# Kernel optimization log

Hardware: AMD Instinct MI355X
Metric: run time of the kernel (lower is better)

The kernel has to match this reference:

```python
import jax, jax.numpy as jnp
import numpy as np

B, N, DIM, H, DH = 8, 1024, 768, 12, 64
INNER = H * DH
SCALE = DH ** -0.5


def _bias_idx(n):
    # Reproduce the offset->id mapping from the torch __init__ loop:
    # offsets are first seen in row-major (p1, p2) order, so
    # id(0)=0, id(-k)=k (k=1..n-1), id(+k)=n-1+k.
    i = np.arange(n)[:, None]
    j = np.arange(n)[None, :]
    off = i - j
    idx = np.where(off <= 0, -off, n - 1 + off)
    return jnp.asarray(idx, dtype=jnp.int32)  # (n, n), values in [0, 2n-2]


def setup_inputs() -> dict:
    key = jax.random.key(0)
    ks = jax.random.split(key, 5)
    x = jax.random.normal(ks[0], (B, N, DIM), dtype=jnp.float32)
    w_qkv = jax.random.normal(ks[1], (DIM, 3 * INNER), dtype=jnp.float32) * (DIM ** -0.5)
    bias_table = jax.random.normal(ks[2], (H, 2 * N - 1), dtype=jnp.float32) * 0.02
    w_out = jax.random.normal(ks[3], (INNER, DIM), dtype=jnp.float32) * (INNER ** -0.5)
    b_out = jnp.zeros((DIM,), dtype=jnp.float32)
    bias_idx = _bias_idx(N)
    return {"x": x, "w_qkv": w_qkv, "bias_table": bias_table,
            "w_out": w_out, "b_out": b_out, "bias_idx": bias_idx}


def reference(x, w_qkv, bias_table, w_out, b_out, bias_idx):
    b, n, _ = x.shape
    qkv = x @ w_qkv  # (b, n, 3*inner)
    q, k, v = jnp.split(qkv, 3, axis=-1)
    def heads(t):
        return t.reshape(b, n, H, DH).transpose(0, 2, 1, 3)  # (b, h, n, d)
    q, k, v = heads(q), heads(k), heads(v)
    bias = bias_table[:, bias_idx]  # (h, n, n), gathered per-head relpos bias
    dots = jnp.einsum('bhid,bhjd->bhij', q, k) * SCALE + bias[None]
    attn = jax.nn.softmax(dots, axis=-1)
    out = jnp.einsum('bhij,bhjd->bhid', attn, v)
    out = out.transpose(0, 2, 1, 3).reshape(b, n, INNER)
    return out @ w_out + b_out
```

## Files before the change

kernel.cpp:

```cpp
#include <hip/hip_runtime.h>
#include <hip/hip_bf16.h>
#include <stdint.h>

typedef unsigned short u16;
typedef unsigned int u32;
typedef __bf16 bf16x8 __attribute__((ext_vector_type(8)));
typedef _Float16 f16x8 __attribute__((ext_vector_type(8)));
typedef _Float16 f16x4 __attribute__((ext_vector_type(4)));
typedef __fp16 v4hf __attribute__((ext_vector_type(4)));
typedef float f32x4 __attribute__((ext_vector_type(4)));
typedef unsigned short u16x4 __attribute__((ext_vector_type(4)));
typedef unsigned int u32x2 __attribute__((ext_vector_type(2)));

#define SEQ     1024
#define DIM     768
#define NH      12
#define QKV_LD  2304
#define LOG2E   1.4426950408889634f
#define C1      0.18033688f

__device__ __forceinline__ float bf2f(u16 u) {
    union { unsigned v; float f; } x; x.v = ((unsigned)u) << 16; return x.f;
}
__device__ __forceinline__ u16 f2bf(float f) {
    union { float f; unsigned v; } x; x.f = f;
    unsigned r = (x.v + 0x7FFFu + ((x.v >> 16) & 1u)) >> 16;
    return (u16)r;
}
__device__ __forceinline__ void store_out(u16* p, float v)  { *p = f2bf(v); }
__device__ __forceinline__ void store_out(float* p, float v){ *p = v; }

__device__ __forceinline__ void async16(void* lds, const void* g) {
    __builtin_amdgcn_global_load_lds(
        (const __attribute__((address_space(1))) unsigned*)(uintptr_t)g,
        (__attribute__((address_space(3))) unsigned*)(unsigned)(uintptr_t)lds,
        16, 0, 0);
}

__global__ __launch_bounds__(256) void cvt_k(const float* __restrict__ in,
                                             u16* __restrict__ out) {
    int i = (blockIdx.x * 256 + threadIdx.x) * 4;
    float4 v = *(const float4*)(in + i);
    u16x4 o = { f2bf(v.x), f2bf(v.y), f2bf(v.z), f2bf(v.w) };
    *(u16x4*)(out + i) = o;
}

__global__ __launch_bounds__(256) void transpose_k(const float* __restrict__ in,
                                                   u16* __restrict__ out,
                                                   int R, int C) {
    __shared__ __align__(16) float t[32][33];
    int c0 = blockIdx.x * 32, r0 = blockIdx.y * 32;
    int tx = threadIdx.x & 31, ty = threadIdx.x >> 5;
#pragma unroll
    for (int i = 0; i < 32; i += 8)
        t[ty + i][tx] = in[(size_t)(r0 + ty + i) * C + c0 + tx];
    __syncthreads();
#pragma unroll
    for (int i = 0; i < 32; i += 8)
        out[(size_t)(c0 + ty + i) * R + r0 + tx] = f2bf(t[tx][ty + i]);
}

__global__ __launch_bounds__(256) void vt_k(const u16* __restrict__ qkv,
                                            _Float16* __restrict__ vT) {
    __shared__ __align__(16) u16 t[32][33];
    int bh = blockIdx.z;
    int b = bh / 12, h = bh % 12;
    int key0 = blockIdx.x * 32, dh0 = blockIdx.y * 32;
    int tx = threadIdx.x & 31, ty = threadIdx.x >> 5;
#pragma unroll
    for (int i = 0; i < 32; i += 8)
        t[ty + i][tx] = qkv[(size_t)(b * SEQ + key0 + ty + i) * QKV_LD +
                            1536 + h * 64 + dh0 + tx];
    __syncthreads();
#pragma unroll
    for (int i = 0; i < 32; i += 8)
        vT[(size_t)(bh * 64 + dh0 + ty + i) * SEQ + key0 + tx] =
            (_Float16)bf2f(t[tx][ty + i]);
}

template <int HAS_BIAS, typename OUT_T>
__global__ __launch_bounds__(256) void gemm_bt(const u16* __restrict__ A,
                                               const u16* __restrict__ Bt,
                                               const float* __restrict__ bias,
                                               OUT_T* __restrict__ C,
                                               int M, int N, int K) {
    __shared__ __align__(16) u16 sA[128 * 64];
    __shared__ __align__(16) u16 sB[128 * 64];
    const int tid = threadIdx.x;
    const int lane = tid & 63;
    const int quad = lane >> 4, l16 = lane & 15;
    const int wave = tid >> 6;
    const int m0 = blockIdx.x * 128, n0 = blockIdx.y * 128;
    const int wm = (wave >> 1) * 64, wn = (wave & 1) * 64;

    const int co0 = (quad ^ (l16 & 7)) * 8;
    f32x4 acc[4][4] = {};

    for (int k0 = 0; k0 < K; k0 += 64) {
        __syncthreads();
#pragma unroll
        for (int rep = 0; rep < 4; ++rep) {
            int i = rep * 256 + tid;
            int row = i >> 3;
            int c = (i & 7) ^ (row & 7);
            async16(&sA[i * 8], A + (size_t)(m0 + row) * K + k0 + c * 8);
            async16(&sB[i * 8], Bt + (size_t)(n0 + row) * K + k0 + c * 8);
        }
        __syncthreads();

#pragma unroll
        for (int ks = 0; ks < 2; ++ks) {
            const int co = co0 ^ (ks * 32);
            bf16x8 af[4], bfr[4];
#pragma unroll
            for (int mi = 0; mi < 4; ++mi)
                af[mi] = *(const bf16x8*)&sA[(wm + mi * 16 + l16) * 64 + co];
#pragma unroll
            for (int nj = 0; nj < 4; ++nj)
                bfr[nj] = *(const bf16x8*)&sB[(wn + nj * 16 + l16) * 64 + co];
#pragma unroll
            for (int mi = 0; mi < 4; ++mi)
#pragma unroll
                for (int nj = 0; nj < 4; ++nj)
                    acc[mi][nj] = __builtin_amdgcn_mfma_f32_16x16x32_bf16(
                        af[mi], bfr[nj], acc[mi][nj], 0, 0, 0);
        }
    }

#pragma unroll
    for (int mi = 0; mi < 4; ++mi) {
#pragma unroll
        for (int nj = 0; nj < 4; ++nj) {
            int col = n0 + wn + nj * 16 + l16;
            float bv = HAS_BIAS ? bias[col] : 0.0f;
#pragma unroll
            for (int r = 0; r < 4; ++r) {
                int row = m0 + wm + mi * 16 + quad * 4 + r;
                store_out(&C[(size_t)row * N + col], acc[mi][nj][r] + bv);
            }
        }
    }
}

__global__ __launch_bounds__(256) void attn_k(const u16* __restrict__ qkv,
                                              const _Float16* __restrict__ vT,
                                              const float* __restrict__ bias_table,
                                              u16* __restrict__ out) {
    __shared__ __align__(16) u16 sK[2][64 * 64];
    __shared__ __align__(16) _Float16 sV[2][64 * 64];
    __shared__ __align__(16) float sLut[2048];

    const int tid = threadIdx.x;
    const int wave = tid >> 6, lane = tid & 63;
    const int quad = lane >> 4, l16 = lane & 15;
    const int bh = blockIdx.x;
    const int b = bh / NH, h = bh % NH;
    const int q0 = blockIdx.y * 128, wq = wave * 32;

    for (int i = tid; i < 2047; i += 256)
        sLut[i] = LOG2E * bias_table[h * 2047 + (i <= 1023 ? 1023 - i : i)];

    bf16x8 qf[2][2];
#pragma unroll
    for (int nt = 0; nt < 2; ++nt)
#pragma unroll
        for (int hf = 0; hf < 2; ++hf)
            qf[nt][hf] = *(const bf16x8*)(qkv +
                (size_t)(b * SEQ + q0 + wq + nt * 16 + l16) * QKV_LD +
                h * 64 + hf * 32 + quad * 8);

    const u16* kg[2];
    const _Float16* vg[2];
    int lds_i[2];
#pragma unroll
    for (int rep = 0; rep < 2; ++rep) {
        int i = rep * 256 + wave * 64 + lane;
        int row = i >> 3;
        int c = (i & 7) ^ (row & 7);
        kg[rep] = qkv + (size_t)(b * SEQ + row) * QKV_LD + 768 + h * 64 + c * 8;
        vg[rep] = vT + (size_t)(bh * 64 + row) * SEQ + c * 8;
        lds_i[rep] = i * 8;
    }

    const int co0 = (quad ^ (l16 & 7)) * 8;
    const int co1 = co0 ^ 32;
    int voff[4];
#pragma unroll
    for (int mt = 0; mt < 4; ++mt)
        voff[mt] = (((mt * 2 + (quad >> 1)) ^ (l16 & 7)) * 8) + (quad & 1) * 4;
    const int ib0 = q0 + wq + l16 - quad * 4 + 1023;

#pragma unroll
    for (int rep = 0; rep < 2; ++rep) {
        async16(&sK[0][lds_i[rep]], kg[rep]);
        async16(&sV[0][lds_i[rep]], vg[rep]);
        kg[rep] += (size_t)64 * QKV_LD;
        vg[rep] += 64;
    }
    __syncthreads();

    f32x4 o[2][4] = {};
    f32x4 osum[2] = {};
    const u32x2 onebits = { 0x3C003C00u, 0x3C003C00u };
    const v4hf ones = __builtin_bit_cast(v4hf, onebits);

    for (int kt = 0; kt < SEQ / 64; ++kt) {
        const int cur = kt & 1;
        if (kt + 1 < SEQ / 64) {
            const int nxt = cur ^ 1;
#pragma unroll
            for (int rep = 0; rep < 2; ++rep) {
                async16(&sK[nxt][lds_i[rep]], kg[rep]);
                async16(&sV[nxt][lds_i[rep]], vg[rep]);
                kg[rep] += (size_t)64 * QKV_LD;
                vg[rep] += 64;
            }
        }
        const u16* sKc = sK[cur];
        const _Float16* sVc = sV[cur];
        const int ibk = ib0 - kt * 64;

        v4hf pfrag[4][2];
#pragma unroll
        for (int mt = 0; mt < 4; ++mt) {
            const u16* kr = sKc + mt * 1024 + l16 * 64;
            bf16x8 af0 = *(const bf16x8*)(kr + co0);
            bf16x8 af1 = *(const bf16x8*)(kr + co1);
#pragma unroll
            for (int nt = 0; nt < 2; ++nt) {
                f32x4 s = {0.f, 0.f, 0.f, 0.f};
                s = __builtin_amdgcn_mfma_f32_16x16x32_bf16(af0, qf[nt][0], s, 0, 0, 0);
                s = __builtin_amdgcn_mfma_f32_16x16x32_bf16(af1, qf[nt][1], s, 0, 0, 0);
                const float* bw = &sLut[ibk + nt * 16 - mt * 16];
                float p[4];
#pragma unroll
                for (int r = 0; r < 4; ++r)
                    p[r] = __builtin_amdgcn_exp2f(s[r] * C1 + bw[-r]);
                u32 lo = __builtin_bit_cast(u32, __builtin_amdgcn_cvt_pkrtz(p[0], p[1]));
                u32 hi = __builtin_bit_cast(u32, __builtin_amdgcn_cvt_pkrtz(p[2], p[3]));
                u32x2 pk = { lo, hi };
                pfrag[mt][nt] = __builtin_bit_cast(v4hf, pk);
            }
        }

#pragma unroll
        for (int mt = 0; mt < 4; ++mt) {
#pragma unroll
            for (int nt = 0; nt < 2; ++nt)
                osum[nt] = __builtin_amdgcn_mfma_f32_16x16x16f16(
                    ones, pfrag[mt][nt], osum[nt], 0, 0, 0);
        }
#pragma unroll
        for (int c4 = 0; c4 < 4; ++c4) {
            const _Float16* vr = sVc + (c4 * 16 + l16) * 64;
#pragma unroll
            for (int mt = 0; mt < 4; ++mt) {
                v4hf va = __builtin_bit_cast(v4hf, *(const f16x4*)(vr + voff[mt]));
#pragma unroll
                for (int nt = 0; nt < 2; ++nt)
                    o[nt][c4] = __builtin_amdgcn_mfma_f32_16x16x16f16(
                        va, pfrag[mt][nt], o[nt][c4], 0, 0, 0);
            }
        }
        __syncthreads();
    }

#pragma unroll
    for (int nt = 0; nt < 2; ++nt) {
        float inv = __builtin_amdgcn_rcpf(osum[nt][0]);
        size_t rowbase = (size_t)(b * SEQ + q0 + wq + nt * 16 + l16) * DIM + h * 64;
#pragma unroll
        for (int c4 = 0; c4 < 4; ++c4) {
            u16x4 pk = { f2bf(o[nt][c4][0] * inv), f2bf(o[nt][c4][1] * inv),
                         f2bf(o[nt][c4][2] * inv), f2bf(o[nt][c4][3] * inv) };
            *(u16x4*)&out[rowbase + c4 * 16 + quad * 4] = pk;
        }
    }
}

extern "C" void kernel_launch(void* const* d_in, const int* in_sizes, int n_in,
                              void* d_out, int out_size, void* d_ws, size_t ws_size,
                              hipStream_t stream) {
    const float* x          = (const float*)d_in[0];
    const float* w_qkv      = (const float*)d_in[1];
    const float* bias_table = (const float*)d_in[2];
    const float* w_out      = (const float*)d_in[3];
    const float* b_out      = (const float*)d_in[4];
    float* out = (float*)d_out;

    char* ws = (char*)d_ws;
    u16* ws_qkv        = (u16*)(ws);
    u16* ws_attn       = (u16*)(ws + 37748736);
    u16* ws_xb         = (u16*)(ws + 50331648);
    u16* ws_wqkvT      = (u16*)(ws + 62914560);
    u16* ws_woutT      = (u16*)(ws + 66453504);
    _Float16* ws_vT    = (_Float16*)(ws + 67633152);

    cvt_k<<<8 * 1024 * 768 / 1024, 256, 0, stream>>>(x, ws_xb);
    transpose_k<<<dim3(2304 / 32, 768 / 32), 256, 0, stream>>>(w_qkv, ws_wqkvT, 768, 2304);
    transpose_k<<<dim3(768 / 32, 768 / 32), 256, 0, stream>>>(w_out, ws_woutT, 768, 768);

    gemm_bt<0, u16><<<dim3(8192 / 128, 2304 / 128), 256, 0, stream>>>(
        ws_xb, ws_wqkvT, nullptr, ws_qkv, 8192, 2304, 768);

    vt_k<<<dim3(SEQ / 32, 2, 8 * NH), 256, 0, stream>>>(ws_qkv, ws_vT);

    attn_k<<<dim3(8 * NH, SEQ / 128, 1), 256, 0, stream>>>(ws_qkv, ws_vT, bias_table, ws_attn);

    gemm_bt<1, float><<<dim3(8192 / 128, 768 / 128), 256, 0, stream>>>(
        ws_attn, ws_woutT, b_out, out, 8192, 768, 768);
}
```

Baseline: 195.0 us.

## Switch attention kernel to 32x32 MFMA tiles with permlane32 fragment shuffles

Rewrites the attention inner loop so QK^T, the row-sum and PV use 32x32x16 MFMA instructions instead of 16x16 ones. The probability tile is repacked into B-operand layout with permlane32_swap, so no LDS round trip is needed. This cuts the MFMA issue count and the LDS fragment loads per tile. It also sets launch bounds to three blocks per CU. The larger accumulators raise register pressure, and the new lane mapping and swizzle indexing must stay correct.

```diff
diff --git a/kernel.cpp b/kernel.cpp
--- a/kernel.cpp
+++ b/kernel.cpp
@@ -6,11 +6,10 @@
 typedef unsigned int u32;
 typedef __bf16 bf16x8 __attribute__((ext_vector_type(8)));
 typedef _Float16 f16x8 __attribute__((ext_vector_type(8)));
-typedef _Float16 f16x4 __attribute__((ext_vector_type(4)));
-typedef __fp16 v4hf __attribute__((ext_vector_type(4)));
 typedef float f32x4 __attribute__((ext_vector_type(4)));
+typedef float f32x16 __attribute__((ext_vector_type(16)));
 typedef unsigned short u16x4 __attribute__((ext_vector_type(4)));
-typedef unsigned int u32x2 __attribute__((ext_vector_type(2)));
+typedef unsigned int u32x4 __attribute__((ext_vector_type(4)));
 
 #define SEQ     1024
 #define DIM     768
@@ -142,17 +141,17 @@
     }
 }
 
-__global__ __launch_bounds__(256) void attn_k(const u16* __restrict__ qkv,
-                                              const _Float16* __restrict__ vT,
-                                              const float* __restrict__ bias_table,
-                                              u16* __restrict__ out) {
+__global__ __launch_bounds__(256, 3) void attn_k(const u16* __restrict__ qkv,
+                                                 const _Float16* __restrict__ vT,
+                                                 const float* __restrict__ bias_table,
+                                                 u16* __restrict__ out) {
     __shared__ __align__(16) u16 sK[2][64 * 64];
     __shared__ __align__(16) _Float16 sV[2][64 * 64];
     __shared__ __align__(16) float sLut[2048];
 
     const int tid = threadIdx.x;
     const int wave = tid >> 6, lane = tid & 63;
-    const int quad = lane >> 4, l16 = lane & 15;
+    const int l31 = lane & 31, hi = lane >> 5;
     const int bh = blockIdx.x;
     const int b = bh / NH, h = bh % NH;
     const int q0 = blockIdx.y * 128, wq = wave * 32;
@@ -160,49 +159,41 @@
     for (int i = tid; i < 2047; i += 256)
         sLut[i] = LOG2E * bias_table[h * 2047 + (i <= 1023 ? 1023 - i : i)];
 
-    bf16x8 qf[2][2];
-#pragma unroll
-    for (int nt = 0; nt < 2; ++nt)
-#pragma unroll
-        for (int hf = 0; hf < 2; ++hf)
-            qf[nt][hf] = *(const bf16x8*)(qkv +
-                (size_t)(b * SEQ + q0 + wq + nt * 16 + l16) * QKV_LD +
-                h * 64 + hf * 32 + quad * 8);
-
-    const u16* kg[2];
-    const _Float16* vg[2];
+    bf16x8 qf[4];
+#pragma unroll
+    for (int ks = 0; ks < 4; ++ks)
+        qf[ks] = *(const bf16x8*)(qkv +
+            (size_t)(b * SEQ + q0 + wq + l31) * QKV_LD + h * 64 + ks * 16 + hi * 8);
+
+    const u16* kgp[2];
+    const _Float16* vgp[2];
     int lds_i[2];
 #pragma unroll
     for (int rep = 0; rep < 2; ++rep) {
         int i = rep * 256 + wave * 64 + lane;
         int row = i >> 3;
         int c = (i & 7) ^ (row & 7);
-        kg[rep] = qkv + (size_t)(b * SEQ + row) * QKV_LD + 768 + h * 64 + c * 8;
-        vg[rep] = vT + (size_t)(bh * 64 + row) * SEQ + c * 8;
+        kgp[rep] = qkv + (size_t)(b * SEQ + row) * QKV_LD + 768 + h * 64 + c * 8;
+        vgp[rep] = vT + (size_t)(bh * 64 + row) * SEQ + c * 8;
         lds_i[rep] = i * 8;
     }
 
-    const int co0 = (quad ^ (l16 & 7)) * 8;
-    const int co1 = co0 ^ 32;
-    int voff[4];
-#pragma unroll
-    for (int mt = 0; mt < 4; ++mt)
-        voff[mt] = (((mt * 2 + (quad >> 1)) ^ (l16 & 7)) * 8) + (quad & 1) * 4;
-    const int ib0 = q0 + wq + l16 - quad * 4 + 1023;
+    const int ib0 = 1023 + q0 + wq + l31;
+    const int hi4 = hi * 4;
 
 #pragma unroll
     for (int rep = 0; rep < 2; ++rep) {
-        async16(&sK[0][lds_i[rep]], kg[rep]);
-        async16(&sV[0][lds_i[rep]], vg[rep]);
-        kg[rep] += (size_t)64 * QKV_LD;
-        vg[rep] += 64;
+        async16(&sK[0][lds_i[rep]], kgp[rep]);
+        async16(&sV[0][lds_i[rep]], vgp[rep]);
+        kgp[rep] += (size_t)64 * QKV_LD;
+        vgp[rep] += 64;
     }
     __syncthreads();
 
-    f32x4 o[2][4] = {};
-    f32x4 osum[2] = {};
-    const u32x2 onebits = { 0x3C003C00u, 0x3C003C00u };
-    const v4hf ones = __builtin_bit_cast(v4hf, onebits);
+    f32x16 o[2] = {};
+    f32x16 osum = {};
+    const u32x4 onebits = { 0x3C003C00u, 0x3C003C00u, 0x3C003C00u, 0x3C003C00u };
+    const f16x8 ones = __builtin_bit_cast(f16x8, onebits);
 
     for (int kt = 0; kt < SEQ / 64; ++kt) {
         const int cur = kt & 1;
@@ -210,70 +201,74 @@
             const int nxt = cur ^ 1;
 #pragma unroll
             for (int rep = 0; rep < 2; ++rep) {
-                async16(&sK[nxt][lds_i[rep]], kg[rep]);
-                async16(&sV[nxt][lds_i[rep]], vg[rep]);
-                kg[rep] += (size_t)64 * QKV_LD;
-                vg[rep] += 64;
+                async16(&sK[nxt][lds_i[rep]], kgp[rep]);
+                async16(&sV[nxt][lds_i[rep]], vgp[rep]);
+                kgp[rep] += (size_t)64 * QKV_LD;
+                vgp[rep] += 64;
             }
         }
         const u16* sKc = sK[cur];
         const _Float16* sVc = sV[cur];
-        const int ibk = ib0 - kt * 64;
-
-        v4hf pfrag[4][2];
-#pragma unroll
-        for (int mt = 0; mt < 4; ++mt) {
-            const u16* kr = sKc + mt * 1024 + l16 * 64;
-            bf16x8 af0 = *(const bf16x8*)(kr + co0);
-            bf16x8 af1 = *(const bf16x8*)(kr + co1);
-#pragma unroll
-            for (int nt = 0; nt < 2; ++nt) {
-                f32x4 s = {0.f, 0.f, 0.f, 0.f};
-                s = __builtin_amdgcn_mfma_f32_16x16x32_bf16(af0, qf[nt][0], s, 0, 0, 0);
-                s = __builtin_amdgcn_mfma_f32_16x16x32_bf16(af1, qf[nt][1], s, 0, 0, 0);
-                const float* bw = &sLut[ibk + nt * 16 - mt * 16];
-                float p[4];
-#pragma unroll
-                for (int r = 0; r < 4; ++r)
-                    p[r] = __builtin_amdgcn_exp2f(s[r] * C1 + bw[-r]);
-                u32 lo = __builtin_bit_cast(u32, __builtin_amdgcn_cvt_pkrtz(p[0], p[1]));
-                u32 hi = __builtin_bit_cast(u32, __builtin_amdgcn_cvt_pkrtz(p[2], p[3]));
-                u32x2 pk = { lo, hi };
-                pfrag[mt][nt] = __builtin_bit_cast(v4hf, pk);
-            }
-        }
-
-#pragma unroll
-        for (int mt = 0; mt < 4; ++mt) {
-#pragma unroll
-            for (int nt = 0; nt < 2; ++nt)
-                osum[nt] = __builtin_amdgcn_mfma_f32_16x16x16f16(
-                    ones, pfrag[mt][nt], osum[nt], 0, 0, 0);
-        }
-#pragma unroll
-        for (int c4 = 0; c4 < 4; ++c4) {
-            const _Float16* vr = sVc + (c4 * 16 + l16) * 64;
-#pragma unroll
-            for (int mt = 0; mt < 4; ++mt) {
-                v4hf va = __builtin_bit_cast(v4hf, *(const f16x4*)(vr + voff[mt]));
-#pragma unroll
-                for (int nt = 0; nt < 2; ++nt)
-                    o[nt][c4] = __builtin_amdgcn_mfma_f32_16x16x16f16(
-                        va, pfrag[mt][nt], o[nt][c4], 0, 0, 0);
+
+        f16x8 pfrag[4];
+#pragma unroll
+        for (int t = 0; t < 2; ++t) {
+            const u16* kr = sKc + (t * 32 + l31) * 64;
+            f32x16 s = {};
+#pragma unroll
+            for (int ks = 0; ks < 4; ++ks) {
+                int slot = (2 * ks + hi) ^ (l31 & 7);
+                bf16x8 af = *(const bf16x8*)(kr + slot * 8);
+                s = __builtin_amdgcn_mfma_f32_32x32x16_bf16(af, qf[ks], s, 0, 0, 0);
+            }
+            const int ibt = ib0 - kt * 64 - t * 32 - hi4;
+            u32 wlo[4], whi[4];
+#pragma unroll
+            for (int g = 0; g < 4; ++g) {
+                const float* bw = &sLut[ibt - 8 * g];
+                float p0 = __builtin_amdgcn_exp2f(s[4 * g + 0] * C1 + bw[0]);
+                float p1 = __builtin_amdgcn_exp2f(s[4 * g + 1] * C1 + bw[-1]);
+                float p2 = __builtin_amdgcn_exp2f(s[4 * g + 2] * C1 + bw[-2]);
+                float p3 = __builtin_amdgcn_exp2f(s[4 * g + 3] * C1 + bw[-3]);
+                wlo[g] = __builtin_bit_cast(u32, __builtin_amdgcn_cvt_pkrtz(p0, p1));
+                whi[g] = __builtin_bit_cast(u32, __builtin_amdgcn_cvt_pkrtz(p2, p3));
+            }
+#pragma unroll
+            for (int c = 0; c < 2; ++c) {
+                auto rlo = __builtin_amdgcn_permlane32_swap(
+                    wlo[2 * c], wlo[2 * c + 1], false, false);
+                auto rhi = __builtin_amdgcn_permlane32_swap(
+                    whi[2 * c], whi[2 * c + 1], false, false);
+                u32x4 f = { rlo[0], rhi[0], rlo[1], rhi[1] };
+                pfrag[t * 2 + c] = __builtin_bit_cast(f16x8, f);
+            }
+        }
+
+#pragma unroll
+        for (int kg = 0; kg < 4; ++kg)
+            osum = __builtin_amdgcn_mfma_f32_32x32x16_f16(ones, pfrag[kg], osum, 0, 0, 0);
+#pragma unroll
+        for (int dt = 0; dt < 2; ++dt) {
+            const _Float16* vr = sVc + (dt * 32 + l31) * 64;
+#pragma unroll
+            for (int kg = 0; kg < 4; ++kg) {
+                int slot = (2 * kg + hi) ^ (l31 & 7);
+                f16x8 vf = *(const f16x8*)(vr + slot * 8);
+                o[dt] = __builtin_amdgcn_mfma_f32_32x32x16_f16(vf, pfrag[kg], o[dt], 0, 0, 0);
             }
         }
         __syncthreads();
     }
 
-#pragma unroll
-    for (int nt = 0; nt < 2; ++nt) {
-        float inv = __builtin_amdgcn_rcpf(osum[nt][0]);
-        size_t rowbase = (size_t)(b * SEQ + q0 + wq + nt * 16 + l16) * DIM + h * 64;
-#pragma unroll
-        for (int c4 = 0; c4 < 4; ++c4) {
-            u16x4 pk = { f2bf(o[nt][c4][0] * inv), f2bf(o[nt][c4][1] * inv),
-                         f2bf(o[nt][c4][2] * inv), f2bf(o[nt][c4][3] * inv) };
-            *(u16x4*)&out[rowbase + c4 * 16 + quad * 4] = pk;
+    float inv = __builtin_amdgcn_rcpf(osum[0]);
+    size_t rowbase = (size_t)(b * SEQ + q0 + wq + l31) * DIM + h * 64 + hi4;
+#pragma unroll
+    for (int dt = 0; dt < 2; ++dt) {
+#pragma unroll
+        for (int g = 0; g < 4; ++g) {
+            u16x4 pk = { f2bf(o[dt][4 * g + 0] * inv), f2bf(o[dt][4 * g + 1] * inv),
+                         f2bf(o[dt][4 * g + 2] * inv), f2bf(o[dt][4 * g + 3] * inv) };
+            *(u16x4*)&out[rowbase + dt * 32 + 8 * g] = pk;
         }
     }
 }
```

After: 198.6 us. About the same (+1.8%).
